# Performance work log

Measured on AMD Instinct MI355X. Metric: run time of the kernel, lower is better.

## Reference

```python
import jax, jax.numpy as jnp
import numpy as np

N_SCOPE, N_HOLE, S, D, H, L = 2048, 512, 64, 256, 8, 4
HD = D // H
VOCAB, FREQ, NUM_RANKS = 2048, 500, 4
NEG = -1e9


def _ln(x, s, b):
    m = x.mean(-1, keepdims=True)
    v = ((x - m) ** 2).mean(-1, keepdims=True)
    return (x - m) * jax.lax.rsqrt(v + 1e-5) * s + b


def _pos_enc(pos):
    # sinusoidal positional encoding with base freq 500 -> [N, D]
    i = jnp.arange(D // 2, dtype=jnp.float32)
    ang = pos.astype(jnp.float32)[:, None] / (FREQ ** (2.0 * i / D))
    return jnp.concatenate([jnp.sin(ang), jnp.cos(ang)], axis=-1)


def _embed(tokens, emb):
    # sum of per-field embeddings, tokens [N,S,3] -> [N,S,D]
    return emb[0][tokens[..., 0]] + emb[1][tokens[..., 1]] + emb[2][tokens[..., 2]]


def _encoder(x, pad, Wq, Wk, Wv, Wo, ln1_s, ln1_b, W1, b1, W2, b2, ln2_s, ln2_b):
    # post-norm transformer stack; pad [N,S] True = valid
    mask = jnp.where(pad[:, None, None, :], 0.0, NEG)  # [N,1,1,S]
    for l in range(L):
        q = (x @ Wq[l]).reshape(*x.shape[:2], H, HD)
        k = (x @ Wk[l]).reshape(*x.shape[:2], H, HD)
        v = (x @ Wv[l]).reshape(*x.shape[:2], H, HD)
        scores = jnp.einsum('nqhd,nkhd->nhqk', q, k) / jnp.sqrt(jnp.float32(HD))
        atn = jax.nn.softmax(scores + mask, axis=-1)
        o = jnp.einsum('nhqk,nkhd->nqhd', atn, v).reshape(*x.shape[:2], D) @ Wo[l]
        x = _ln(x + o, ln1_s[l], ln1_b[l])
        h = jax.nn.relu(x @ W1[l] + b1[l]) @ W2[l] + b2[l]
        x = _ln(x + h, ln2_s[l], ln2_b[l])
    return x


def _term_encode(feats, pad, refmask, refids, storage, params):
    # dense_features[reference_mask] = reference_storage[reference_ids]
    x = jnp.where(refmask[..., None], storage[refids], feats)
    x = _encoder(x, pad, *params)
    return x[:, 0]  # CLS


def setup_inputs() -> dict:
    key = jax.random.key(0)
    k = jax.random.split(key, 16)
    tokens_scope = jax.random.randint(k[0], (N_SCOPE, S, 3), 0, VOCAB, dtype=jnp.int32)
    tokens_hole = jax.random.randint(k[1], (N_HOLE, S, 3), 0, VOCAB, dtype=jnp.int32)
    pad_scope = jax.random.bernoulli(k[2], 0.8, (N_SCOPE, S)).at[:, 0].set(True)
    pad_hole = jax.random.bernoulli(k[3], 0.8, (N_HOLE, S)).at[:, 0].set(True)
    ref_scope = jax.random.bernoulli(k[4], 0.1, (N_SCOPE, S))
    ref_hole = jax.random.bernoulli(k[5], 0.1, (N_HOLE, S))
    scope_sort = jax.random.randint(k[6], (N_SCOPE,), 0, NUM_RANKS, dtype=jnp.int32)
    scope_positions = jax.random.randint(k[7], (N_SCOPE,), 0, FREQ, dtype=jnp.int32)
    sd = D ** -0.5
    return dict(
        tokens_scope=tokens_scope, tokens_hole=tokens_hole,
        pad_scope=pad_scope, pad_hole=pad_hole,
        ref_scope=ref_scope, ref_hole=ref_hole,
        scope_sort=scope_sort, scope_positions=scope_positions,
        emb=jax.random.normal(k[8], (3, VOCAB, D)) * 0.02,
        Wq=jax.random.normal(k[9], (L, D, D)) * sd,
        Wk=jax.random.normal(k[10], (L, D, D)) * sd,
        Wv=jax.random.normal(k[11], (L, D, D)) * sd,
        Wo=jax.random.normal(k[12], (L, D, D)) * sd,
        ln1_s=jnp.ones((L, D)), ln1_b=jnp.zeros((L, D)),
        W1=jax.random.normal(k[13], (L, D, 4 * D)) * sd,
        b1=jnp.zeros((L, 4 * D)),
        W2=jax.random.normal(k[14], (L, 4 * D, D)) * (4 * D) ** -0.5,
        b2=jnp.zeros((L, D)),
        ln2_s=jnp.ones((L, D)), ln2_b=jnp.zeros((L, D)),
    )


def reference(tokens_scope, tokens_hole, pad_scope, pad_hole, ref_scope, ref_hole,
              scope_sort, scope_positions, emb, Wq, Wk, Wv, Wo,
              ln1_s, ln1_b, W1, b1, W2, b2, ln2_s, ln2_b):
    params = (Wq, Wk, Wv, Wo, ln1_s, ln1_b, W1, b1, W2, b2, ln2_s, ln2_b)
    scope_feats = _embed(tokens_scope, emb)   # [Ns,S,D]
    hole_feats = _embed(tokens_hole, emb)     # [Nh,S,D]
    scope_reprs = _pos_enc(scope_positions)   # [Ns,D]
    # iterate dependency ranks; attention is per-term so computing over all
    # terms and masking the additive update is identical to the torch loop
    for rank in range(NUM_RANKS):
        enc = _term_encode(scope_feats, pad_scope, ref_scope,
                           tokens_scope[:, :, 1], scope_reprs, params)
        rank_mask = (scope_sort == rank)[:, None]
        scope_reprs = scope_reprs + jnp.where(rank_mask, enc, 0.0)
    hole_reprs = _term_encode(hole_feats, pad_hole, ref_hole,
                              tokens_hole[:, :, 1], scope_reprs, params)
    return scope_reprs, hole_reprs
```

## Files before the change

kernel.cpp:

```cpp
#include <hip/hip_runtime.h>
#include <stdint.h>
#include <math.h>

typedef __attribute__((ext_vector_type(8))) short bf16x8;
typedef __attribute__((ext_vector_type(4))) short s16x4;
typedef __attribute__((ext_vector_type(4))) float f32x4;
typedef unsigned short u16;

#define SBAR() asm volatile("s_waitcnt lgkmcnt(0)\ns_barrier" ::: "memory")

__device__ __forceinline__ short f2bf(float f){
  union { float f; uint32_t u; } v; v.f = f;
  uint32_t r = v.u + 0x7FFFu + ((v.u >> 16) & 1u);
  return (short)(r >> 16);
}
__device__ __forceinline__ float bf2f(u16 b){
  union { uint32_t u; float f; } v; v.u = ((uint32_t)b) << 16; return v.f;
}
__device__ __forceinline__ bool getb(const void* p, int i, int flag){
  if (flag) return ((const unsigned char*)p)[i] != 0;
  return ((const int*)p)[i] != 0;
}
__device__ __forceinline__ int xoff(int row, int col){
  int g = (col >> 3) ^ (row & 7);
  return row * 256 + (g << 3) + (col & 7);
}

__global__ void detect_bool_k(const void* pad, int* flag){
  const unsigned char* b = (const unsigned char*)pad;
  int f = 0;
  for (int i = 1; i < 64; ++i) if (i & 3) f |= (b[i] != 0) ? 1 : 0;
  *flag = f;
}

__global__ void pack_k(const float* __restrict__ src, u16* __restrict__ dst, int K, int N){
  long idx = (long)blockIdx.x * blockDim.x + threadIdx.x;
  int j = (int)(idx & 7);
  int lane = (int)((idx >> 3) & 63);
  long t = idx >> 9;
  int KT = K >> 5;
  int kt = (int)(t % KT);
  long t2 = t / KT;
  int NT = N >> 4;
  int nt = (int)(t2 % NT);
  int m = (int)(t2 / NT);
  int li = lane & 15, lg = lane >> 4;
  int k = 32*kt + 8*lg + j, n = 16*nt + li;
  dst[idx] = (u16)f2bf(src[((long)m * K + k) * N + n]);
}

__global__ void emb2bf_k(const float* __restrict__ src, u16* __restrict__ dst){
  long i = (long)blockIdx.x * blockDim.x + threadIdx.x;
  dst[i] = (u16)f2bf(src[i]);
}

__global__ void pos_init_k(const int* __restrict__ pos, float* __restrict__ reprs){
  int n = blockIdx.x, d = threadIdx.x;
  double p = (double)pos[n];
  int i = (d < 128) ? d : d - 128;
  double ang = p / pow(500.0, (2.0 * (double)i) / 256.0);
  reprs[n * 256 + d] = (d < 128) ? (float)sin(ang) : (float)cos(ang);
}

__global__ void zero_counts_k(int* c){ if (threadIdx.x < 4) c[threadIdx.x] = 0; }

__global__ void compact_k(const int* __restrict__ sortv, int* __restrict__ lists,
                          int* __restrict__ counts){
  int t = blockIdx.x * 256 + threadIdx.x;
  int r = sortv[t];
  int pos = atomicAdd(&counts[r], 1);
  lists[r * 2048 + pos] = t;
}

__global__ void update_k(const int* __restrict__ sortv, const float* __restrict__ encCLS,
                         float* __restrict__ reprs, int rank){
  int t = blockIdx.x;
  if (sortv[t] != rank) return;
  reprs[t * 256 + threadIdx.x] += encCLS[t * 256 + threadIdx.x];
}

__global__ void writeout_k(const float* __restrict__ reprs, float* __restrict__ out){
  int i = blockIdx.x * 256 + threadIdx.x;
  out[i] = reprs[i];
}

__global__ __launch_bounds__(512, 2)
void encode_k(const int* __restrict__ tokens, const void* __restrict__ pad,
              const void* __restrict__ refm, const int* __restrict__ boolflag,
              const float* __restrict__ storage, const u16* __restrict__ embB,
              const u16* __restrict__ WqF, const u16* __restrict__ WkF,
              const u16* __restrict__ WvF, const u16* __restrict__ WoF,
              const u16* __restrict__ W1F, const float* __restrict__ b1,
              const u16* __restrict__ W2F, const float* __restrict__ b2,
              const float* __restrict__ ln1s, const float* __restrict__ ln1b,
              const float* __restrict__ ln2s, const float* __restrict__ ln2b,
              const int* __restrict__ list, const int* __restrict__ cnt,
              float* __restrict__ outCLS)
{
  int term;
  if (list){
    if ((int)blockIdx.x >= *cnt) return;
    term = list[blockIdx.x];
  } else {
    term = blockIdx.x;
  }
  const int flag = *boolflag;

  __shared__ u16 sXb[64 * 256];
  __shared__ u16 sPoolA[64 * 136];
  __shared__ u16 sPoolB[64 * 72 * 2];
  __shared__ u16 sPbuf[2 * 64 * 72];
  __shared__ float sStat[64][8];
  __shared__ float sMask[64];
  __shared__ int sTok[192];
  __shared__ int sRef[64];

  u16 (*sQK)[136] = (u16(*)[136])sPoolA;
  u16 (*sVT)[72]  = (u16(*)[72])sPoolB;
  u16 (*sO)[72]   = (u16(*)[72])(sPoolB + 64*72);
  u16 (*sH0)[136] = (u16(*)[136])sPoolA;
  u16 (*sH1)[136] = (u16(*)[136])sPbuf;

  const int tid = threadIdx.x;
  const int w = tid >> 6, lane = tid & 63, lg = lane >> 4, li = lane & 15;
  const int wr = w >> 2, wc = w & 3;
  const int rbase = 32 * wr;
  const f32x4 zero4 = {0.f, 0.f, 0.f, 0.f};

  if (tid < 192) sTok[tid] = tokens[term * 192 + tid];
  if (tid < 64){
    sMask[tid] = getb(pad, term * 64 + tid, flag) ? 0.f : -1e9f;
    sRef[tid] = getb(refm, term * 64 + tid, flag) ? 1 : 0;
  }
  SBAR();

  {
    int col = tid & 255, rh = tid >> 8;
    #pragma unroll 4
    for (int s = 32*rh; s < 32*rh + 32; ++s){
      float v;
      if (sRef[s]){
        v = storage[sTok[3*s + 1] * 256 + col];
      } else {
        v = bf2f(embB[sTok[3*s + 0] * 256 + col])
          + bf2f(embB[(2048 + sTok[3*s + 1]) * 256 + col])
          + bf2f(embB[(4096 + sTok[3*s + 2]) * 256 + col]);
      }
      sXb[xoff(s, col)] = (u16)f2bf(v);
    }
  }
  SBAR();

  float xres[2][4][4];
  #pragma unroll
  for (int rt = 0; rt < 2; ++rt)
    #pragma unroll
    for (int ctl = 0; ctl < 4; ++ctl)
      #pragma unroll
      for (int r = 0; r < 4; ++r)
        xres[rt][ctl][r] = bf2f(sXb[xoff(rbase + 16*rt + 4*lg + r, 64*wc + 16*ctl + li)]);

  auto ldA = [&](int rt, int kk) -> bf16x8 {
    return *(const bf16x8*)&sXb[(rbase + 16*rt + li) * 256 + (((4*kk + lg) ^ (li & 7)) << 3)];
  };

  for (int l = 0; l < 4; ++l){
    f32x4 ga[2][4];
    #pragma unroll
    for (int rt = 0; rt < 2; ++rt)
      #pragma unroll
      for (int c = 0; c < 4; ++c) ga[rt][c] = zero4;

    for (int hp = 0; hp < 4; ++hp){
      f32x4 acc[2][3];
      #pragma unroll
      for (int rt = 0; rt < 2; ++rt)
        #pragma unroll
        for (int c = 0; c < 3; ++c) acc[rt][c] = zero4;

      const u16* bF[3];
      #pragma unroll
      for (int ctl = 0; ctl < 3; ++ctl){
        int c = 48 * wc + 16 * ctl;
        int mm = c >> 6;
        int nt = hp * 4 + ((c & 63) >> 4);
        const u16* Wt = (mm == 0) ? WqF : ((mm == 1) ? WkF : WvF);
        bF[ctl] = Wt + (((size_t)(l * 16 + nt) * 8) * 64 + lane) * 8;
      }
      bf16x8 bq[8][3];
      #pragma unroll
      for (int kt = 0; kt < 8; ++kt)
        #pragma unroll
        for (int ctl = 0; ctl < 3; ++ctl)
          bq[kt][ctl] = *(const bf16x8*)(bF[ctl] + (size_t)kt * 512);
      #pragma unroll
      for (int kt = 0; kt < 8; ++kt){
        bf16x8 a[2];
        #pragma unroll
        for (int rt = 0; rt < 2; ++rt) a[rt] = ldA(rt, kt);
        #pragma unroll
        for (int ctl = 0; ctl < 3; ++ctl)
          #pragma unroll
          for (int rt = 0; rt < 2; ++rt)
            acc[rt][ctl] = __builtin_amdgcn_mfma_f32_16x16x32_bf16(a[rt], bq[kt][ctl], acc[rt][ctl], 0, 0, 0);
      }
      #pragma unroll
      for (int rt = 0; rt < 2; ++rt)
        #pragma unroll
        for (int ctl = 0; ctl < 3; ++ctl){
          int c = 48*wc + 16*ctl;
          if (c < 128){
            #pragma unroll
            for (int r = 0; r < 4; ++r)
              sQK[rbase + 16*rt + 4*lg + r][c + li] = (u16)f2bf(acc[rt][ctl][r]);
          } else {
            s16x4 pk;
            #pragma unroll
            for (int r = 0; r < 4; ++r) pk[r] = f2bf(acc[rt][ctl][r]);
            *(s16x4*)&sVT[c + li - 128][rbase + 16*rt + 4*lg] = pk;
          }
        }
      bf16x8 woB[2][4];
      #pragma unroll
      for (int kt2 = 0; kt2 < 2; ++kt2)
        #pragma unroll
        for (int ctl = 0; ctl < 4; ++ctl)
          woB[kt2][ctl] = *(const bf16x8*)(WoF +
              (((size_t)(l*16 + 4*wc + ctl) * 8 + 2*hp + kt2) * 64 + lane) * 8);
      SBAR();

      {
        const int hh = wr, qs = wc;
        u16 (*sP)[72] = (u16(*)[72])(sPbuf + hh * 64 * 72);
        bf16x8 aq = *(const bf16x8*)&sQK[16*qs + li][32*hh + 8*lg];
        f32x4 sc[4];
        #pragma unroll
        for (int ct = 0; ct < 4; ++ct){
          bf16x8 bk = *(const bf16x8*)&sQK[16*ct + li][64 + 32*hh + 8*lg];
          sc[ct] = __builtin_amdgcn_mfma_f32_16x16x32_bf16(aq, bk, zero4, 0, 0, 0);
        }
        float sv[4][4];
        #pragma unroll
        for (int ct = 0; ct < 4; ++ct){
          float mk = sMask[16*ct + li];
          #pragma unroll
          for (int r = 0; r < 4; ++r) sv[ct][r] = sc[ct][r] * 0.17677669529663687f + mk;
        }
        #pragma unroll
        for (int r = 0; r < 4; ++r){
          float m = fmaxf(fmaxf(sv[0][r], sv[1][r]), fmaxf(sv[2][r], sv[3][r]));
          #pragma unroll
          for (int o = 1; o < 16; o <<= 1) m = fmaxf(m, __shfl_xor(m, o, 64));
          float s0 = 0.f;
          #pragma unroll
          for (int ct = 0; ct < 4; ++ct){ float e = __expf(sv[ct][r] - m); sv[ct][r] = e; s0 += e; }
          #pragma unroll
          for (int o = 1; o < 16; o <<= 1) s0 += __shfl_xor(s0, o, 64);
          float inv = 1.f / s0;
          #pragma unroll
          for (int ct = 0; ct < 4; ++ct) sv[ct][r] *= inv;
        }
        #pragma unroll
        for (int ct = 0; ct < 4; ++ct)
          #pragma unroll
          for (int r = 0; r < 4; ++r)
            sP[16*qs + 4*lg + r][16*ct + li] = (u16)f2bf(sv[ct][r]);
        f32x4 oa[2] = {zero4, zero4};
        #pragma unroll
        for (int kt = 0; kt < 2; ++kt){
          bf16x8 ap = *(const bf16x8*)&sP[16*qs + li][32*kt + 8*lg];
          #pragma unroll
          for (int ct = 0; ct < 2; ++ct){
            bf16x8 bv = *(const bf16x8*)&sVT[32*hh + 16*ct + li][32*kt + 8*lg];
            oa[ct] = __builtin_amdgcn_mfma_f32_16x16x32_bf16(ap, bv, oa[ct], 0, 0, 0);
          }
        }
        #pragma unroll
        for (int ct = 0; ct < 2; ++ct)
          #pragma unroll
          for (int r = 0; r < 4; ++r)
            sO[16*qs + 4*lg + r][32*hh + 16*ct + li] = (u16)f2bf(oa[ct][r]);
      }
      SBAR();
      #pragma unroll
      for (int kt2 = 0; kt2 < 2; ++kt2){
        bf16x8 a[2];
        #pragma unroll
        for (int rt = 0; rt < 2; ++rt)
          a[rt] = *(const bf16x8*)&sO[rbase + 16*rt + li][32*kt2 + 8*lg];
        #pragma unroll
        for (int ctl = 0; ctl < 4; ++ctl)
          #pragma unroll
          for (int rt = 0; rt < 2; ++rt)
            ga[rt][ctl] = __builtin_amdgcn_mfma_f32_16x16x32_bf16(a[rt], woB[kt2][ctl], ga[rt][ctl], 0, 0, 0);
      }
    }

    {
      float g4[4], bb4[4];
      #pragma unroll
      for (int ctl = 0; ctl < 4; ++ctl){
        int col = 64*wc + 16*ctl + li;
        g4[ctl] = ln1s[l*256 + col]; bb4[ctl] = ln1b[l*256 + col];
      }
      float s1v[2][4], s2v[2][4];
      #pragma unroll
      for (int rt = 0; rt < 2; ++rt)
        #pragma unroll
        for (int r = 0; r < 4; ++r){
          float t1 = 0.f, t2 = 0.f;
          #pragma unroll
          for (int ctl = 0; ctl < 4; ++ctl){
            float y = ga[rt][ctl][r] + xres[rt][ctl][r];
            ga[rt][ctl][r] = y; t1 += y; t2 += y * y;
          }
          #pragma unroll
          for (int o = 1; o < 16; o <<= 1){ t1 += __shfl_xor(t1, o, 64); t2 += __shfl_xor(t2, o, 64); }
          s1v[rt][r] = t1; s2v[rt][r] = t2;
        }
      if (li == 0){
        #pragma unroll
        for (int rt = 0; rt < 2; ++rt)
          #pragma unroll
          for (int r = 0; r < 4; ++r){
            sStat[rbase + 16*rt + 4*lg + r][wc] = s1v[rt][r];
            sStat[rbase + 16*rt + 4*lg + r][4 + wc] = s2v[rt][r];
          }
      }
      SBAR();
      #pragma unroll
      for (int rt = 0; rt < 2; ++rt)
        #pragma unroll
        for (int r = 0; r < 4; ++r){
          int row = rbase + 16*rt + 4*lg + r;
          float su = sStat[row][0] + sStat[row][1] + sStat[row][2] + sStat[row][3];
          float sq = sStat[row][4] + sStat[row][5] + sStat[row][6] + sStat[row][7];
          float mean = su * (1.f / 256.f);
          float var = sq * (1.f / 256.f) - mean * mean;
          float rs = rsqrtf(var + 1e-5f);
          #pragma unroll
          for (int ctl = 0; ctl < 4; ++ctl){
            int col = 64*wc + 16*ctl + li;
            float nv = (ga[rt][ctl][r] - mean) * rs * g4[ctl] + bb4[ctl];
            xres[rt][ctl][r] = nv;
            sXb[xoff(row, col)] = (u16)f2bf(nv);
          }
        }
      SBAR();
    }

    {
      float b1v[8][2];
      #pragma unroll
      for (int ch = 0; ch < 8; ++ch)
        #pragma unroll
        for (int ctl = 0; ctl < 2; ++ctl)
          b1v[ch][ctl] = b1[l*1024 + 128*ch + 32*wc + 16*ctl + li];

      bf16x8 w1f[2][8];
      auto loadW1 = [&](int ch){
        #pragma unroll
        for (int ctl = 0; ctl < 2; ++ctl){
          const u16* p0 = W1F + (((size_t)(l*64 + 8*ch + 2*wc + ctl) * 8) * 64 + lane) * 8;
          #pragma unroll
          for (int kt = 0; kt < 8; ++kt)
            w1f[ctl][kt] = *(const bf16x8*)(p0 + (size_t)kt * 512);
        }
      };
      auto mfma1 = [&](f32x4 (*h)[2]){
        #pragma unroll
        for (int rt = 0; rt < 2; ++rt){ h[rt][0] = zero4; h[rt][1] = zero4; }
        #pragma unroll
        for (int kt = 0; kt < 8; ++kt){
          bf16x8 a[2];
          #pragma unroll
          for (int rt = 0; rt < 2; ++rt) a[rt] = ldA(rt, kt);
          #pragma unroll
          for (int ctl = 0; ctl < 2; ++ctl)
            #pragma unroll
            for (int rt = 0; rt < 2; ++rt)
              h[rt][ctl] = __builtin_amdgcn_mfma_f32_16x16x32_bf16(a[rt], w1f[ctl][kt], h[rt][ctl], 0, 0, 0);
        }
      };

      f32x4 fa[2][4];
      #pragma unroll
      for (int rt = 0; rt < 2; ++rt)
        #pragma unroll
        for (int c = 0; c < 4; ++c) fa[rt][c] = zero4;

      f32x4 haA[2][2], haB[2][2];
      loadW1(0);
      mfma1(haA);

      #pragma unroll
      for (int ch = 0; ch < 8; ++ch){
        f32x4 (*cur)[2] = (ch & 1) ? haB : haA;
        f32x4 (*nxt)[2] = (ch & 1) ? haA : haB;
        u16 (*sHc)[136] = (ch & 1) ? sH1 : sH0;
        #pragma unroll
        for (int rt = 0; rt < 2; ++rt)
          #pragma unroll
          for (int ctl = 0; ctl < 2; ++ctl)
            #pragma unroll
            for (int r = 0; r < 4; ++r){
              float v = cur[rt][ctl][r] + b1v[ch][ctl];
              sHc[rbase + 16*rt + 4*lg + r][32*wc + 16*ctl + li] = (u16)f2bf(fmaxf(v, 0.f));
            }
        bf16x8 w2a[2][4];
        #pragma unroll
        for (int kt = 0; kt < 2; ++kt)
          #pragma unroll
          for (int ctl = 0; ctl < 4; ++ctl)
            w2a[kt][ctl] = *(const bf16x8*)(W2F +
                (((size_t)(l*16 + 4*wc + ctl) * 32 + 4*ch + kt) * 64 + lane) * 8);
        SBAR();
        if (ch < 7) loadW1(ch + 1);
        #pragma unroll
        for (int kt = 0; kt < 2; ++kt){
          bf16x8 a[2];
          #pragma unroll
          for (int rt = 0; rt < 2; ++rt)
            a[rt] = *(const bf16x8*)&sHc[rbase + 16*rt + li][32*kt + 8*lg];
          #pragma unroll
          for (int ctl = 0; ctl < 4; ++ctl)
            #pragma unroll
            for (int rt = 0; rt < 2; ++rt)
              fa[rt][ctl] = __builtin_amdgcn_mfma_f32_16x16x32_bf16(a[rt], w2a[kt][ctl], fa[rt][ctl], 0, 0, 0);
        }
        #pragma unroll
        for (int kt = 2; kt < 4; ++kt){
          bf16x8 br[4];
          #pragma unroll
          for (int ctl = 0; ctl < 4; ++ctl)
            br[ctl] = *(const bf16x8*)(W2F +
                (((size_t)(l*16 + 4*wc + ctl) * 32 + 4*ch + kt) * 64 + lane) * 8);
          bf16x8 a[2];
          #pragma unroll
          for (int rt = 0; rt < 2; ++rt)
            a[rt] = *(const bf16x8*)&sHc[rbase + 16*rt + li][32*kt + 8*lg];
          #pragma unroll
          for (int ctl = 0; ctl < 4; ++ctl)
            #pragma unroll
            for (int rt = 0; rt < 2; ++rt)
              fa[rt][ctl] = __builtin_amdgcn_mfma_f32_16x16x32_bf16(a[rt], br[ctl], fa[rt][ctl], 0, 0, 0);
        }
        if (ch < 7) mfma1(nxt);
      }

      float g4[4], bb4[4], b2v[4];
      #pragma unroll
      for (int ctl = 0; ctl < 4; ++ctl){
        int col = 64*wc + 16*ctl + li;
        g4[ctl] = ln2s[l*256 + col]; bb4[ctl] = ln2b[l*256 + col]; b2v[ctl] = b2[l*256 + col];
      }
      float s1v[2][4], s2v[2][4];
      #pragma unroll
      for (int rt = 0; rt < 2; ++rt)
        #pragma unroll
        for (int r = 0; r < 4; ++r){
          float t1 = 0.f, t2 = 0.f;
          #pragma unroll
          for (int ctl = 0; ctl < 4; ++ctl){
            float y = fa[rt][ctl][r] + xres[rt][ctl][r] + b2v[ctl];
            fa[rt][ctl][r] = y; t1 += y; t2 += y * y;
          }
          #pragma unroll
          for (int o = 1; o < 16; o <<= 1){ t1 += __shfl_xor(t1, o, 64); t2 += __shfl_xor(t2, o, 64); }
          s1v[rt][r] = t1; s2v[rt][r] = t2;
        }
      if (li == 0){
        #pragma unroll
        for (int rt = 0; rt < 2; ++rt)
          #pragma unroll
          for (int r = 0; r < 4; ++r){
            sStat[rbase + 16*rt + 4*lg + r][wc] = s1v[rt][r];
            sStat[rbase + 16*rt + 4*lg + r][4 + wc] = s2v[rt][r];
          }
      }
      SBAR();
      #pragma unroll
      for (int rt = 0; rt < 2; ++rt)
        #pragma unroll
        for (int r = 0; r < 4; ++r){
          int row = rbase + 16*rt + 4*lg + r;
          float su = sStat[row][0] + sStat[row][1] + sStat[row][2] + sStat[row][3];
          float sq = sStat[row][4] + sStat[row][5] + sStat[row][6] + sStat[row][7];
          float mean = su * (1.f / 256.f);
          float var = sq * (1.f / 256.f) - mean * mean;
          float rs = rsqrtf(var + 1e-5f);
          #pragma unroll
          for (int ctl = 0; ctl < 4; ++ctl){
            int col = 64*wc + 16*ctl + li;
            float nv = (fa[rt][ctl][r] - mean) * rs * g4[ctl] + bb4[ctl];
            xres[rt][ctl][r] = nv;
            sXb[xoff(row, col)] = (u16)f2bf(nv);
            if (l == 3 && outCLS && row == 0) outCLS[term * 256 + col] = nv;
          }
        }
      SBAR();
    }
  }
}

extern "C" void kernel_launch(void* const* d_in, const int* in_sizes, int n_in,
                              void* d_out, int out_size, void* d_ws, size_t ws_size,
                              hipStream_t stream)
{
  (void)in_sizes; (void)n_in; (void)out_size; (void)ws_size;
  const int* tokens_scope = (const int*)d_in[0];
  const int* tokens_hole  = (const int*)d_in[1];
  const void* pad_scope = d_in[2];
  const void* pad_hole  = d_in[3];
  const void* ref_scope = d_in[4];
  const void* ref_hole  = d_in[5];
  const int* scope_sort = (const int*)d_in[6];
  const int* scope_pos  = (const int*)d_in[7];
  const float* emb  = (const float*)d_in[8];
  const float* Wq   = (const float*)d_in[9];
  const float* Wk   = (const float*)d_in[10];
  const float* Wv   = (const float*)d_in[11];
  const float* Wo   = (const float*)d_in[12];
  const float* ln1s = (const float*)d_in[13];
  const float* ln1b = (const float*)d_in[14];
  const float* W1   = (const float*)d_in[15];
  const float* b1   = (const float*)d_in[16];
  const float* W2   = (const float*)d_in[17];
  const float* b2   = (const float*)d_in[18];
  const float* ln2s = (const float*)d_in[19];
  const float* ln2b = (const float*)d_in[20];

  char* p = (char*)d_ws;
  float* reprs  = (float*)p; p += (size_t)2048*256*4;
  float* encCLS = (float*)p; p += (size_t)2048*256*4;
  u16* WqF = (u16*)p; p += (size_t)4*256*256*2;
  u16* WkF = (u16*)p; p += (size_t)4*256*256*2;
  u16* WvF = (u16*)p; p += (size_t)4*256*256*2;
  u16* WoF = (u16*)p; p += (size_t)4*256*256*2;
  u16* W1F = (u16*)p; p += (size_t)4*256*1024*2;
  u16* W2F = (u16*)p; p += (size_t)4*256*1024*2;
  u16* embB = (u16*)p; p += (size_t)3*2048*256*2;
  int* lists = (int*)p; p += (size_t)4*2048*4;
  int* counts = (int*)p; p += 64;
  int* flag = (int*)p; p += 16;

  hipLaunchKernelGGL(detect_bool_k, dim3(1), dim3(1), 0, stream, pad_scope, flag);
  hipLaunchKernelGGL(emb2bf_k, dim3(6144), dim3(256), 0, stream, emb, embB);
  hipLaunchKernelGGL(pack_k, dim3(1024), dim3(256), 0, stream, Wq, WqF, 256, 256);
  hipLaunchKernelGGL(pack_k, dim3(1024), dim3(256), 0, stream, Wk, WkF, 256, 256);
  hipLaunchKernelGGL(pack_k, dim3(1024), dim3(256), 0, stream, Wv, WvF, 256, 256);
  hipLaunchKernelGGL(pack_k, dim3(1024), dim3(256), 0, stream, Wo, WoF, 256, 256);
  hipLaunchKernelGGL(pack_k, dim3(4096), dim3(256), 0, stream, W1, W1F, 256, 1024);
  hipLaunchKernelGGL(pack_k, dim3(4096), dim3(256), 0, stream, W2, W2F, 1024, 256);
  hipLaunchKernelGGL(pos_init_k, dim3(2048), dim3(256), 0, stream, scope_pos, reprs);
  hipLaunchKernelGGL(zero_counts_k, dim3(1), dim3(64), 0, stream, counts);
  hipLaunchKernelGGL(compact_k, dim3(8), dim3(256), 0, stream, scope_sort, lists, counts);

  for (int r = 0; r < 4; ++r){
    hipLaunchKernelGGL(encode_k, dim3(2048), dim3(512), 0, stream,
      tokens_scope, pad_scope, ref_scope, flag, reprs, embB,
      WqF, WkF, WvF, WoF, W1F, b1, W2F, b2, ln1s, ln1b, ln2s, ln2b,
      lists + (size_t)r*2048, counts + r, encCLS);
    hipLaunchKernelGGL(update_k, dim3(2048), dim3(256), 0, stream, scope_sort, encCLS, reprs, r);
  }
  hipLaunchKernelGGL(encode_k, dim3(512), dim3(512), 0, stream,
      tokens_hole, pad_hole, ref_hole, flag, reprs, embB,
      WqF, WkF, WvF, WoF, W1F, b1, W2F, b2, ln1s, ln1b, ln2s, ln2b,
      (const int*)nullptr, (const int*)nullptr, (float*)d_out + (size_t)2048*256);
  hipLaunchKernelGGL(writeout_k, dim3(2048), dim3(256), 0, stream, reprs, (float*)d_out);
}
```

Measured before the change: 2.795 ms.

## Shrink LDS footprint with swizzled buffers, register softmax, raise occupancy

Replaces the padded LDS arrays with XOR-swizzled unpadded buffers and aliases the token, ref and stat scratch into the pooled buffers. The pad mask moves from LDS into a wave ballot. The attention probability matrix no longer goes through shared memory: QK^T is computed transposed so each lane holds its softmax columns, and P is redistributed with ds_bpermute. Together these cut LDS use so launch bounds can target 4 blocks per CU instead of 2. The cost is register pressure under the tighter bound and one extra barrier after the FFN.

```diff
diff --git a/kernel.cpp b/kernel.cpp
--- a/kernel.cpp
+++ b/kernel.cpp
@@ -1,6 +1,7 @@
 #include <hip/hip_runtime.h>
 #include <stdint.h>
 #include <math.h>
+#include <string.h>
 
 typedef __attribute__((ext_vector_type(8))) short bf16x8;
 typedef __attribute__((ext_vector_type(4))) short s16x4;
@@ -22,8 +23,13 @@
   return ((const int*)p)[i] != 0;
 }
 __device__ __forceinline__ int xoff(int row, int col){
-  int g = (col >> 3) ^ (row & 7);
-  return row * 256 + (g << 3) + (col & 7);
+  return row * 256 + ((((col >> 3) ^ (row & 7))) << 3) + (col & 7);
+}
+__device__ __forceinline__ int swz128(int row, int col){
+  return row * 128 + (((col >> 3) ^ (row & 7)) << 3) + (col & 7);
+}
+__device__ __forceinline__ int swz64(int row, int col){
+  return row * 64 + (((col >> 3) ^ (row & 7)) << 3) + (col & 7);
 }
 
 __global__ void detect_bool_k(const void* pad, int* flag){
@@ -84,7 +90,7 @@
   out[i] = reprs[i];
 }
 
-__global__ __launch_bounds__(512, 2)
+__global__ __launch_bounds__(512, 4)
 void encode_k(const int* __restrict__ tokens, const void* __restrict__ pad,
               const void* __restrict__ refm, const int* __restrict__ boolflag,
               const float* __restrict__ storage, const u16* __restrict__ embB,
@@ -107,19 +113,17 @@
   const int flag = *boolflag;
 
   __shared__ u16 sXb[64 * 256];
-  __shared__ u16 sPoolA[64 * 136];
-  __shared__ u16 sPoolB[64 * 72 * 2];
-  __shared__ u16 sPbuf[2 * 64 * 72];
-  __shared__ float sStat[64][8];
-  __shared__ float sMask[64];
-  __shared__ int sTok[192];
-  __shared__ int sRef[64];
-
-  u16 (*sQK)[136] = (u16(*)[136])sPoolA;
-  u16 (*sVT)[72]  = (u16(*)[72])sPoolB;
-  u16 (*sO)[72]   = (u16(*)[72])(sPoolB + 64*72);
-  u16 (*sH0)[136] = (u16(*)[136])sPoolA;
-  u16 (*sH1)[136] = (u16(*)[136])sPbuf;
+  __shared__ u16 sPoolA[64 * 128];
+  __shared__ u16 sPoolB[64 * 128];
+
+  u16* sQK = sPoolA;
+  u16* sVT = sPoolB;
+  u16* sO  = sPoolB + 64 * 64;
+  u16* sH0 = sPoolA;
+  u16* sH1 = sPoolB;
+  float (*sStat)[8] = (float(*)[8])sPoolB;
+  int* sTok = (int*)sPoolA;
+  int* sRef = sTok + 192;
 
   const int tid = threadIdx.x;
   const int w = tid >> 6, lane = tid & 63, lg = lane >> 4, li = lane & 15;
@@ -128,10 +132,8 @@
   const f32x4 zero4 = {0.f, 0.f, 0.f, 0.f};
 
   if (tid < 192) sTok[tid] = tokens[term * 192 + tid];
-  if (tid < 64){
-    sMask[tid] = getb(pad, term * 64 + tid, flag) ? 0.f : -1e9f;
-    sRef[tid] = getb(refm, term * 64 + tid, flag) ? 1 : 0;
-  }
+  if (tid < 64) sRef[tid] = getb(refm, term * 64 + tid, flag) ? 1 : 0;
+  unsigned long long mb = __ballot(getb(pad, term * 64 + lane, flag));
   SBAR();
 
   {
@@ -212,12 +214,12 @@
           if (c < 128){
             #pragma unroll
             for (int r = 0; r < 4; ++r)
-              sQK[rbase + 16*rt + 4*lg + r][c + li] = (u16)f2bf(acc[rt][ctl][r]);
+              sQK[swz128(rbase + 16*rt + 4*lg + r, c + li)] = (u16)f2bf(acc[rt][ctl][r]);
           } else {
-            s16x4 pk;
+            s16x4 pk4;
             #pragma unroll
-            for (int r = 0; r < 4; ++r) pk[r] = f2bf(acc[rt][ctl][r]);
-            *(s16x4*)&sVT[c + li - 128][rbase + 16*rt + 4*lg] = pk;
+            for (int r = 0; r < 4; ++r) pk4[r] = f2bf(acc[rt][ctl][r]);
+            *(s16x4*)&sVT[swz64(c + li - 128, rbase + 16*rt + 4*lg)] = pk4;
           }
         }
       bf16x8 woB[2][4];
@@ -231,55 +233,76 @@
 
       {
         const int hh = wr, qs = wc;
-        u16 (*sP)[72] = (u16(*)[72])(sPbuf + hh * 64 * 72);
-        bf16x8 aq = *(const bf16x8*)&sQK[16*qs + li][32*hh + 8*lg];
+        bf16x8 aq = *(const bf16x8*)&sQK[swz128(16*qs + li, 32*hh + 8*lg)];
         f32x4 sc[4];
         #pragma unroll
         for (int ct = 0; ct < 4; ++ct){
-          bf16x8 bk = *(const bf16x8*)&sQK[16*ct + li][64 + 32*hh + 8*lg];
-          sc[ct] = __builtin_amdgcn_mfma_f32_16x16x32_bf16(aq, bk, zero4, 0, 0, 0);
-        }
-        float sv[4][4];
-        #pragma unroll
-        for (int ct = 0; ct < 4; ++ct){
-          float mk = sMask[16*ct + li];
-          #pragma unroll
-          for (int r = 0; r < 4; ++r) sv[ct][r] = sc[ct][r] * 0.17677669529663687f + mk;
-        }
-        #pragma unroll
-        for (int r = 0; r < 4; ++r){
-          float m = fmaxf(fmaxf(sv[0][r], sv[1][r]), fmaxf(sv[2][r], sv[3][r]));
-          #pragma unroll
-          for (int o = 1; o < 16; o <<= 1) m = fmaxf(m, __shfl_xor(m, o, 64));
-          float s0 = 0.f;
-          #pragma unroll
-          for (int ct = 0; ct < 4; ++ct){ float e = __expf(sv[ct][r] - m); sv[ct][r] = e; s0 += e; }
-          #pragma unroll
-          for (int o = 1; o < 16; o <<= 1) s0 += __shfl_xor(s0, o, 64);
-          float inv = 1.f / s0;
-          #pragma unroll
-          for (int ct = 0; ct < 4; ++ct) sv[ct][r] *= inv;
-        }
+          bf16x8 bk = *(const bf16x8*)&sQK[swz128(16*ct + li, 64 + 32*hh + 8*lg)];
+          sc[ct] = __builtin_amdgcn_mfma_f32_16x16x32_bf16(bk, aq, zero4, 0, 0, 0);
+        }
+        float p[4][4];
         #pragma unroll
         for (int ct = 0; ct < 4; ++ct)
           #pragma unroll
-          for (int r = 0; r < 4; ++r)
-            sP[16*qs + 4*lg + r][16*ct + li] = (u16)f2bf(sv[ct][r]);
+          for (int r = 0; r < 4; ++r){
+            int key = 16*ct + 4*lg + r;
+            float mk = ((mb >> key) & 1ull) ? 0.f : -1e9f;
+            p[ct][r] = sc[ct][r] * 0.17677669529663687f + mk;
+          }
+        float mx = p[0][0];
+        #pragma unroll
+        for (int ct = 0; ct < 4; ++ct)
+          #pragma unroll
+          for (int r = 0; r < 4; ++r) mx = fmaxf(mx, p[ct][r]);
+        mx = fmaxf(mx, __shfl_xor(mx, 16, 64));
+        mx = fmaxf(mx, __shfl_xor(mx, 32, 64));
+        float s0 = 0.f;
+        #pragma unroll
+        for (int ct = 0; ct < 4; ++ct)
+          #pragma unroll
+          for (int r = 0; r < 4; ++r){ float e = __expf(p[ct][r] - mx); p[ct][r] = e; s0 += e; }
+        s0 += __shfl_xor(s0, 16, 64);
+        s0 += __shfl_xor(s0, 32, 64);
+        float inv = 1.f / s0;
+        #pragma unroll
+        for (int ct = 0; ct < 4; ++ct)
+          #pragma unroll
+          for (int r = 0; r < 4; ++r) p[ct][r] *= inv;
+
+        uint32_t pkr[4][2];
+        #pragma unroll
+        for (int ct = 0; ct < 4; ++ct)
+          #pragma unroll
+          for (int h = 0; h < 2; ++h)
+            pkr[ct][h] = (uint32_t)(u16)f2bf(p[ct][2*h])
+                       | ((uint32_t)(u16)f2bf(p[ct][2*h+1]) << 16);
+
         f32x4 oa[2] = {zero4, zero4};
         #pragma unroll
         for (int kt = 0; kt < 2; ++kt){
-          bf16x8 ap = *(const bf16x8*)&sP[16*qs + li][32*kt + 8*lg];
+          uint32_t br[4];
+          #pragma unroll
+          for (int m4 = 0; m4 < 4; ++m4){
+            int srcLane = (((lg & 1) * 2 + (m4 >> 1)) << 4) + li;
+            int lo = __builtin_amdgcn_ds_bpermute(srcLane << 2, (int)pkr[2*kt][m4 & 1]);
+            int hi = __builtin_amdgcn_ds_bpermute(srcLane << 2, (int)pkr[2*kt+1][m4 & 1]);
+            br[m4] = (lg < 2) ? (uint32_t)lo : (uint32_t)hi;
+          }
+          union { uint32_t u[4]; bf16x8 v; } bp;
+          bp.u[0] = br[0]; bp.u[1] = br[1]; bp.u[2] = br[2]; bp.u[3] = br[3];
           #pragma unroll
           for (int ct = 0; ct < 2; ++ct){
-            bf16x8 bv = *(const bf16x8*)&sVT[32*hh + 16*ct + li][32*kt + 8*lg];
-            oa[ct] = __builtin_amdgcn_mfma_f32_16x16x32_bf16(ap, bv, oa[ct], 0, 0, 0);
-          }
-        }
-        #pragma unroll
-        for (int ct = 0; ct < 2; ++ct)
-          #pragma unroll
-          for (int r = 0; r < 4; ++r)
-            sO[16*qs + 4*lg + r][32*hh + 16*ct + li] = (u16)f2bf(oa[ct][r]);
+            bf16x8 av = *(const bf16x8*)&sVT[swz64(32*hh + 16*ct + li, 32*kt + 8*lg)];
+            oa[ct] = __builtin_amdgcn_mfma_f32_16x16x32_bf16(av, bp.v, oa[ct], 0, 0, 0);
+          }
+        }
+        #pragma unroll
+        for (int ct = 0; ct < 2; ++ct){
+          s16x4 o4;
+          #pragma unroll
+          for (int r = 0; r < 4; ++r) o4[r] = f2bf(oa[ct][r]);
+          *(s16x4*)&sO[swz64(16*qs + li, 32*hh + 16*ct + 4*lg)] = o4;
+        }
       }
       SBAR();
       #pragma unroll
@@ -287,7 +310,7 @@
         bf16x8 a[2];
         #pragma unroll
         for (int rt = 0; rt < 2; ++rt)
-          a[rt] = *(const bf16x8*)&sO[rbase + 16*rt + li][32*kt2 + 8*lg];
+          a[rt] = *(const bf16x8*)&sO[swz64(rbase + 16*rt + li, 32*kt2 + 8*lg)];
         #pragma unroll
         for (int ctl = 0; ctl < 4; ++ctl)
           #pragma unroll
@@ -397,7 +420,7 @@
       for (int ch = 0; ch < 8; ++ch){
         f32x4 (*cur)[2] = (ch & 1) ? haB : haA;
         f32x4 (*nxt)[2] = (ch & 1) ? haA : haB;
-        u16 (*sHc)[136] = (ch & 1) ? sH1 : sH0;
+        u16* sHc = (ch & 1) ? sH1 : sH0;
         #pragma unroll
         for (int rt = 0; rt < 2; ++rt)
           #pragma unroll
@@ -405,7 +428,7 @@
             #pragma unroll
             for (int r = 0; r < 4; ++r){
               float v = cur[rt][ctl][r] + b1v[ch][ctl];
-              sHc[rbase + 16*rt + 4*lg + r][32*wc + 16*ctl + li] = (u16)f2bf(fmaxf(v, 0.f));
+              sHc[swz128(rbase + 16*rt + 4*lg + r, 32*wc + 16*ctl + li)] = (u16)f2bf(fmaxf(v, 0.f));
             }
         bf16x8 w2a[2][4];
         #pragma unroll
@@ -421,7 +444,7 @@
           bf16x8 a[2];
           #pragma unroll
           for (int rt = 0; rt < 2; ++rt)
-            a[rt] = *(const bf16x8*)&sHc[rbase + 16*rt + li][32*kt + 8*lg];
+            a[rt] = *(const bf16x8*)&sHc[swz128(rbase + 16*rt + li, 32*kt + 8*lg)];
           #pragma unroll
           for (int ctl = 0; ctl < 4; ++ctl)
             #pragma unroll
@@ -438,7 +461,7 @@
           bf16x8 a[2];
           #pragma unroll
           for (int rt = 0; rt < 2; ++rt)
-            a[rt] = *(const bf16x8*)&sHc[rbase + 16*rt + li][32*kt + 8*lg];
+            a[rt] = *(const bf16x8*)&sHc[swz128(rbase + 16*rt + li, 32*kt + 8*lg)];
           #pragma unroll
           for (int ctl = 0; ctl < 4; ++ctl)
             #pragma unroll
@@ -448,6 +471,7 @@
         if (ch < 7) mfma1(nxt);
       }
 
+      SBAR();
       float g4[4], bb4[4], b2v[4];
       #pragma unroll
       for (int ctl = 0; ctl < 4; ++ctl){
```

New measurement: 5.204 ms. +86.2%, slower.
